# Performance work log

Measured on AMD Instinct MI355X. Metric: run time of the kernel, lower is better.

The kernel has to match this reference:

```python
import jax, jax.numpy as jnp
import numpy as np

B, T, C = 16, 2048, 128
HEAD_SIZE = 128

def setup_inputs() -> dict:
    key = jax.random.key(0)
    k1, k2, k3, k4 = jax.random.split(key, 4)
    x = jax.random.normal(k1, (B, T, C), dtype=jnp.float32)
    # nn.Linear(N_EMBED, head_size, bias=False) weight shape: [head_size, N_EMBED]
    scale = (1.0 / np.sqrt(C)).astype(np.float32)
    Wq = jax.random.normal(k2, (HEAD_SIZE, C), dtype=jnp.float32) * scale
    Wk = jax.random.normal(k3, (HEAD_SIZE, C), dtype=jnp.float32) * scale
    Wv = jax.random.normal(k4, (HEAD_SIZE, C), dtype=jnp.float32) * scale
    return {"x": x, "Wq": Wq, "Wk": Wk, "Wv": Wv}

def reference(x, Wq, Wk, Wv):
    Bd, Td, Cd = x.shape
    q = jnp.einsum('btc,hc->bth', x, Wq)  # [B,T,H]
    k = jnp.einsum('btc,hc->bth', x, Wk)
    v = jnp.einsum('btc,hc->bth', x, Wv)
    # NOTE: original scales by C**-0.5 (embedding dim), not head_size**-0.5
    scores = jnp.einsum('bth,bsh->bts', q, k) * (Cd ** -0.5)  # [B,T,T]
    causal = jnp.tril(jnp.ones((Td, Td), dtype=bool))
    scores = jnp.where(causal, scores, -jnp.inf)
    attn = jax.nn.softmax(scores, axis=-1)
    out = jnp.einsum('bts,bsh->bth', attn, v)  # [B,T,H]
    return out
```

## Files before the change

kernel.cpp:

```cpp
#include <hip/hip_runtime.h>
#include <hip/hip_bf16.h>

#define BB 16
#define TT 2048
#define CC 128
#define HH 128
#define NQT128 16

typedef __bf16 bf16x8 __attribute__((ext_vector_type(8)));
typedef __bf16 bf16x4 __attribute__((ext_vector_type(4)));
typedef float  f32x4  __attribute__((ext_vector_type(4)));
typedef unsigned int u32x2 __attribute__((ext_vector_type(2)));

#define BTH       ((size_t)BB * TT * HH)
#define WBF_OFF   (3 * BTH)

static __device__ __forceinline__ bf16x8 load_cvt8(const float* p) {
    float4 a = *(const float4*)p;
    float4 b = *(const float4*)(p + 4);
    bf16x8 r;
    r[0] = (__bf16)a.x; r[1] = (__bf16)a.y; r[2] = (__bf16)a.z; r[3] = (__bf16)a.w;
    r[4] = (__bf16)b.x; r[5] = (__bf16)b.y; r[6] = (__bf16)b.z; r[7] = (__bf16)b.w;
    return r;
}

static __device__ __forceinline__ void load_lds16(const void* g, void* l) {
    __builtin_amdgcn_global_load_lds(
        (const __attribute__((address_space(1))) unsigned int*)g,
        (__attribute__((address_space(3))) unsigned int*)l, 16, 0, 0);
}

__global__ __launch_bounds__(256) void wcvt_kernel(
    const float* __restrict__ Wq, const float* __restrict__ Wk,
    const float* __restrict__ Wv, __bf16* __restrict__ wbf)
{
    int idx = blockIdx.x * 256 + threadIdx.x;
    int which = idx >> 11;
    int rem = idx & 2047;
    int blk = rem >> 8;
    int r2  = rem & 255;
    int ks   = r2 >> 6;
    int lane = r2 & 63;
    int quad = lane >> 4, l16 = lane & 15;
    const float* src = (which == 0) ? Wq : (which == 1) ? Wk : Wv;
    float sc = (which == 0) ? (0.08838834764831845f * 1.4426950408889634f) : 1.0f;
    const float* p = src + (size_t)(blk * 16 + l16) * CC + ks * 32 + quad * 8;
    bf16x8 v;
    #pragma unroll
    for (int j = 0; j < 8; ++j) v[j] = (__bf16)(p[j] * sc);
    *(bf16x8*)(wbf + (size_t)which * 16384 + (((size_t)(blk * 4 + ks)) << 9) + lane * 8) = v;
}

#define TR_QK 132
#define TR_V  68

__global__ __launch_bounds__(256) void proj_kernel(
    const float* __restrict__ x, __bf16* __restrict__ ws)
{
    __shared__ float  xs[64 * 132];
    __shared__ __bf16 tr[128 * TR_V];

    const int lane = threadIdx.x & 63;
    const int wave = threadIdx.x >> 6;
    const int quad = lane >> 4;
    const int l16  = lane & 15;
    const int tid  = threadIdx.x;
    const int m0 = blockIdx.x * 64;
    const int b  = m0 / TT;
    const int t0 = m0 % TT;

    const __bf16* Wbf = ws + WBF_OFF;
    __bf16* Qs = ws;
    __bf16* Ks = ws + BTH;
    __bf16* Vs = ws + 2 * BTH;

    const float* xg = x + (size_t)m0 * CC;
    #pragma unroll
    for (int t = 0; t < 8; ++t) {
        int f = t * 256 + tid;
        int row = f >> 5, c4 = f & 31;
        float4 v = *(const float4*)(xg + (size_t)f * 4);
        *(float4*)(&xs[row * 132 + c4 * 4]) = v;
    }
    __syncthreads();

    bf16x8 xf[4];
    #pragma unroll
    for (int ks = 0; ks < 4; ++ks)
        xf[ks] = load_cvt8(&xs[(wave * 16 + l16) * 132 + ks * 32 + quad * 8]);

    #pragma unroll
    for (int which = 0; which < 2; ++which) {
        const __bf16* Wb = Wbf + (size_t)which * 16384;
        __bf16* dst = which ? Ks : Qs;
        #pragma unroll
        for (int nt = 0; nt < 8; ++nt) {
            f32x4 acc = {0.f, 0.f, 0.f, 0.f};
            #pragma unroll
            for (int ks = 0; ks < 4; ++ks) {
                bf16x8 wf = *(const bf16x8*)(Wb + (((size_t)(nt * 4 + ks)) << 9) + lane * 8);
                acc = __builtin_amdgcn_mfma_f32_16x16x32_bf16(xf[ks], wf, acc, 0, 0, 0);
            }
            #pragma unroll
            for (int r = 0; r < 4; ++r)
                tr[(wave * 16 + quad * 4 + r) * TR_QK + nt * 16 + l16] = (__bf16)acc[r];
        }
        asm volatile("s_waitcnt lgkmcnt(0)" ::: "memory");
        #pragma unroll
        for (int ks = 0; ks < 4; ++ks) {
            const __bf16* p = &tr[(wave * 16 + l16) * TR_QK + ks * 32 + quad * 8];
            uint2 lo = *(const uint2*)p;
            uint2 hi = *(const uint2*)(p + 4);
            uint4 v; v.x = lo.x; v.y = lo.y; v.z = hi.x; v.w = hi.y;
            __bf16* o = dst + (((size_t)(b * 128 + t0 / 16 + wave) * 4 + ks) << 9) + lane * 8;
            *(uint4*)o = v;
        }
        asm volatile("s_waitcnt lgkmcnt(0)" ::: "memory");
    }

    __syncthreads();
    const __bf16* Wv = Wbf + 2 * 16384;
    #pragma unroll
    for (int msub = 0; msub < 8; ++msub) {
        f32x4 acc = {0.f, 0.f, 0.f, 0.f};
        #pragma unroll
        for (int ks = 0; ks < 4; ++ks) {
            bf16x8 wf = *(const bf16x8*)(Wv + (((size_t)(msub * 4 + ks)) << 9) + lane * 8);
            acc = __builtin_amdgcn_mfma_f32_16x16x32_bf16(wf, xf[ks], acc, 0, 0, 0);
        }
        #pragma unroll
        for (int r = 0; r < 4; ++r)
            tr[(msub * 16 + quad * 4 + r) * TR_V + wave * 16 + l16] = (__bf16)acc[r];
    }
    __syncthreads();
    #pragma unroll
    for (int i = 0; i < 4; ++i) {
        int t32 = i >> 1;
        int h16 = wave * 2 + (i & 1);
        const __bf16* p = &tr[(h16 * 16 + l16) * TR_V + t32 * 32 + quad * 8];
        uint2 lo = *(const uint2*)p;
        uint2 hi = *(const uint2*)(p + 4);
        uint4 v; v.x = lo.x; v.y = lo.y; v.z = hi.x; v.w = hi.y;
        __bf16* o = Vs + (((size_t)(b * 64 + t0 / 32 + t32) * 8 + h16) << 9) + lane * 8;
        *(uint4*)o = v;
    }
}

__global__ __launch_bounds__(256) void attn_kernel(
    const __bf16* __restrict__ ws, float* __restrict__ outp)
{
    __shared__ char ldsBuf[2][24576];

    const int lane = threadIdx.x & 63;
    const int wave = threadIdx.x >> 6;
    const int quad = lane >> 4;
    const int l16  = lane & 15;
    const int lane8 = lane * 8;
    const int lo16 = lane * 16;

    const int lin = blockIdx.x;
    const int b   = (lin & 7) * 2 + ((lin >> 3) & 1);
    const int rest = lin >> 4;
    const int pid  = rest & 7;
    const int hh0  = (rest >> 3) & 1;
    const int mh   = 1 - (rest >> 4);

    const __bf16* Qs = ws;
    const __bf16* Ks = ws + BTH;
    const __bf16* Vs = ws + 2 * BTH;

    const char* kg = (const char*)Ks + (size_t)b * 524288 + wave * 4096 + lo16;
    const char* vg = (const char*)Vs + (size_t)b * 524288 + hh0 * 4096 + wave * 1024 + lo16;

    #define STAGE64(J, BUF)                                                     \
        do {                                                                    \
            char* dK_ = ldsBuf[BUF] + wave * 4096;                              \
            char* dV_ = ldsBuf[BUF] + 16384 + wave * 1024;                      \
            const char* sk_ = kg + (size_t)(J) * 16384;                         \
            _Pragma("unroll")                                                   \
            for (int c_ = 0; c_ < 4; ++c_)                                      \
                load_lds16(sk_ + c_ * 1024, dK_ + c_ * 1024);                   \
            _Pragma("unroll")                                                   \
            for (int h_ = 0; h_ < 2; ++h_)                                      \
                load_lds16(vg + (size_t)(2 * (J) + h_) * 8192, dV_ + h_ * 4096);\
        } while (0)

    #pragma unroll 1
    for (int pass = 0; pass < 2; ++pass) {
        const int qt = pass ? (15 - pid) : pid;
        const int qw = qt * 128 + mh * 64 + wave * 16;
        const int ttw = (qw >> 5) + 1;
        const int nj  = 2 * qt + mh + 1;

        bf16x8 qf[4];
        #pragma unroll
        for (int ks = 0; ks < 4; ++ks)
            qf[ks] = *(const bf16x8*)(Qs + (((size_t)(b * 128 + qt * 8 + mh * 4 + wave) * 4 + ks) << 9) + lane8);

        float l_r = 0.f;
        f32x4 o[4];
        #pragma unroll
        for (int h8 = 0; h8 < 4; ++h8) o[h8] = (f32x4){0.f, 0.f, 0.f, 0.f};

        STAGE64(0, 0);
        asm volatile("s_waitcnt vmcnt(0)" ::: "memory");
        __builtin_amdgcn_s_barrier();

        for (int j = 0; j < nj; ++j) {
            const int cur = j & 1;
            if (j + 1 < nj) STAGE64(j + 1, cur ^ 1);

            #pragma unroll
            for (int half = 0; half < 2; ++half) {
                const int tt = 2 * j + half;
                if (tt >= ttw) continue;
                const char* lk = ldsBuf[cur] + half * 8192;
                const char* lv = ldsBuf[cur] + 16384 + half * 4096;

                f32x4 s2[2];
                #pragma unroll
                for (int nsub = 0; nsub < 2; ++nsub) {
                    bf16x8 kfr[4];
                    #pragma unroll
                    for (int ks = 0; ks < 4; ++ks)
                        kfr[ks] = *(const bf16x8*)(lk + ((nsub * 4 + ks) << 10) + lo16);
                    f32x4 a2 = {0.f, 0.f, 0.f, 0.f};
                    __builtin_amdgcn_s_setprio(1);
                    #pragma unroll
                    for (int ks = 0; ks < 4; ++ks)
                        a2 = __builtin_amdgcn_mfma_f32_16x16x32_bf16(kfr[ks], qf[ks], a2, 0, 0, 0);
                    __builtin_amdgcn_s_setprio(0);
                    s2[nsub] = a2;
                }

                const int k0 = tt * 32;
                unsigned int du[2][2];
                const int qrow = qw + l16;
                if (k0 + 31 > qw) {
                    #pragma unroll
                    for (int nsub = 0; nsub < 2; ++nsub) {
                        const int kb = k0 + nsub * 16 + quad * 4;
                        union { bf16x4 v; unsigned int u[2]; } cv;
                        #pragma unroll
                        for (int r = 0; r < 4; ++r) {
                            float sv = (kb + r > qrow) ? -3e38f : s2[nsub][r];
                            float p = __builtin_amdgcn_exp2f(sv);
                            l_r += p;
                            cv.v[r] = (__bf16)p;
                        }
                        du[nsub][0] = cv.u[0];
                        du[nsub][1] = cv.u[1];
                    }
                } else {
                    #pragma unroll
                    for (int nsub = 0; nsub < 2; ++nsub) {
                        union { bf16x4 v; unsigned int u[2]; } cv;
                        #pragma unroll
                        for (int r = 0; r < 4; ++r) {
                            float p = __builtin_amdgcn_exp2f(s2[nsub][r]);
                            l_r += p;
                            cv.v[r] = (__bf16)p;
                        }
                        du[nsub][0] = cv.u[0];
                        du[nsub][1] = cv.u[1];
                    }
                }

                bf16x8 pf;
                {
                    union { unsigned int u[4]; bf16x8 v; } cc;
                    #pragma unroll
                    for (int h = 0; h < 2; ++h) {
                        u32x2 t1 = __builtin_amdgcn_permlane32_swap(
                            du[0][h], du[1][h], false, false);
                        u32x2 t2 = __builtin_amdgcn_permlane16_swap(
                            t1[0], t1[1], false, false);
                        cc.u[h]     = t2[0];
                        cc.u[2 + h] = t2[1];
                    }
                    pf = cc.v;
                }

                __builtin_amdgcn_s_setprio(1);
                #pragma unroll
                for (int h8 = 0; h8 < 4; ++h8) {
                    bf16x8 v0 = *(const bf16x8*)(lv + (h8 << 10) + lo16);
                    o[h8] = __builtin_amdgcn_mfma_f32_16x16x32_bf16(pf, v0, o[h8], 0, 0, 0);
                }
                __builtin_amdgcn_s_setprio(0);
            }
            asm volatile("s_waitcnt vmcnt(0)" ::: "memory");
            __builtin_amdgcn_s_barrier();
        }

        l_r += __shfl_xor(l_r, 16, 64);
        l_r += __shfl_xor(l_r, 32, 64);
        float inv[4];
        #pragma unroll
        for (int r = 0; r < 4; ++r)
            inv[r] = 1.0f / __shfl(l_r, (lane & 48) | (quad * 4 + r), 64);
        #pragma unroll
        for (int h8 = 0; h8 < 4; ++h8)
            #pragma unroll
            for (int r = 0; r < 4; ++r)
                outp[(size_t)(b * TT + qw + quad * 4 + r) * HH + hh0 * 64 + h8 * 16 + l16] = o[h8][r] * inv[r];
    }
    #undef STAGE64
}

extern "C" void kernel_launch(void* const* d_in, const int* in_sizes, int n_in,
                              void* d_out, int out_size, void* d_ws, size_t ws_size,
                              hipStream_t stream)
{
    const float* x  = (const float*)d_in[0];
    const float* Wq = (const float*)d_in[1];
    const float* Wk = (const float*)d_in[2];
    const float* Wv = (const float*)d_in[3];
    __bf16* ws = (__bf16*)d_ws;
    float* out = (float*)d_out;

    wcvt_kernel<<<24, 256, 0, stream>>>(Wq, Wk, Wv, ws + WBF_OFF);
    proj_kernel<<<512, 256, 0, stream>>>(x, ws);
    attn_kernel<<<512, 256, 0, stream>>>(ws, out);
}
```

Measured before the change: 127.1 us.

## Restructure attention into 2-wave blocks covering one 32-row query tile with full head width

```diff
diff --git a/kernel.cpp b/kernel.cpp
--- a/kernel.cpp
+++ b/kernel.cpp
@@ -146,10 +146,10 @@
     }
 }
 
-__global__ __launch_bounds__(256) void attn_kernel(
+__global__ __launch_bounds__(128) void attn_kernel(
     const __bf16* __restrict__ ws, float* __restrict__ outp)
 {
-    __shared__ char ldsBuf[2][24576];
+    __shared__ char ldsBuf[2][16384];
 
     const int lane = threadIdx.x & 63;
     const int wave = threadIdx.x >> 6;
@@ -160,152 +160,139 @@
 
     const int lin = blockIdx.x;
     const int b   = (lin & 7) * 2 + ((lin >> 3) & 1);
-    const int rest = lin >> 4;
-    const int pid  = rest & 7;
-    const int hh0  = (rest >> 3) & 1;
-    const int mh   = 1 - (rest >> 4);
+    const int kq  = 63 - (lin >> 4);
+    const int qw  = kq * 32 + wave * 16;
+    const int nt  = kq + 1;
 
     const __bf16* Qs = ws;
     const __bf16* Ks = ws + BTH;
     const __bf16* Vs = ws + 2 * BTH;
 
-    const char* kg = (const char*)Ks + (size_t)b * 524288 + wave * 4096 + lo16;
-    const char* vg = (const char*)Vs + (size_t)b * 524288 + hh0 * 4096 + wave * 1024 + lo16;
-
-    #define STAGE64(J, BUF)                                                     \
-        do {                                                                    \
-            char* dK_ = ldsBuf[BUF] + wave * 4096;                              \
-            char* dV_ = ldsBuf[BUF] + 16384 + wave * 1024;                      \
-            const char* sk_ = kg + (size_t)(J) * 16384;                         \
-            _Pragma("unroll")                                                   \
-            for (int c_ = 0; c_ < 4; ++c_)                                      \
-                load_lds16(sk_ + c_ * 1024, dK_ + c_ * 1024);                   \
-            _Pragma("unroll")                                                   \
-            for (int h_ = 0; h_ < 2; ++h_)                                      \
-                load_lds16(vg + (size_t)(2 * (J) + h_) * 8192, dV_ + h_ * 4096);\
+    bf16x8 qf[4];
+    #pragma unroll
+    for (int ks = 0; ks < 4; ++ks)
+        qf[ks] = *(const bf16x8*)(Qs + (((size_t)(b * 128 + 2 * kq + wave) * 4 + ks) << 9) + lane8);
+
+    float l_r = 0.f;
+    f32x4 o[8];
+    #pragma unroll
+    for (int h8 = 0; h8 < 8; ++h8) o[h8] = (f32x4){0.f, 0.f, 0.f, 0.f};
+
+    const char* sbase = (wave ? (const char*)Vs : (const char*)Ks)
+                        + (size_t)b * 524288 + lo16;
+
+    #define STAGE(TTv, BUF)                                        \
+        do {                                                       \
+            const char* s_ = sbase + ((size_t)(TTv) << 13);        \
+            char* d_ = ldsBuf[BUF] + wave * 8192;                  \
+            _Pragma("unroll")                                      \
+            for (int c_ = 0; c_ < 8; ++c_)                         \
+                load_lds16(s_ + c_ * 1024, d_ + c_ * 1024);        \
         } while (0)
 
-    #pragma unroll 1
-    for (int pass = 0; pass < 2; ++pass) {
-        const int qt = pass ? (15 - pid) : pid;
-        const int qw = qt * 128 + mh * 64 + wave * 16;
-        const int ttw = (qw >> 5) + 1;
-        const int nj  = 2 * qt + mh + 1;
-
-        bf16x8 qf[4];
-        #pragma unroll
-        for (int ks = 0; ks < 4; ++ks)
-            qf[ks] = *(const bf16x8*)(Qs + (((size_t)(b * 128 + qt * 8 + mh * 4 + wave) * 4 + ks) << 9) + lane8);
-
-        float l_r = 0.f;
-        f32x4 o[4];
-        #pragma unroll
-        for (int h8 = 0; h8 < 4; ++h8) o[h8] = (f32x4){0.f, 0.f, 0.f, 0.f};
-
-        STAGE64(0, 0);
-        asm volatile("s_waitcnt vmcnt(0)" ::: "memory");
+    STAGE(0, 0);
+
+    for (int tt = 0; tt < nt; ++tt) {
+        const int cur = tt & 1;
+        if (tt + 1 < nt) {
+            STAGE(tt + 1, cur ^ 1);
+            asm volatile("s_waitcnt vmcnt(8)" ::: "memory");
+        } else {
+            asm volatile("s_waitcnt vmcnt(0)" ::: "memory");
+        }
         __builtin_amdgcn_s_barrier();
 
-        for (int j = 0; j < nj; ++j) {
-            const int cur = j & 1;
-            if (j + 1 < nj) STAGE64(j + 1, cur ^ 1);
-
-            #pragma unroll
-            for (int half = 0; half < 2; ++half) {
-                const int tt = 2 * j + half;
-                if (tt >= ttw) continue;
-                const char* lk = ldsBuf[cur] + half * 8192;
-                const char* lv = ldsBuf[cur] + 16384 + half * 4096;
-
-                f32x4 s2[2];
+        const char* lk = ldsBuf[cur];
+        const char* lv = ldsBuf[cur] + 8192;
+
+        f32x4 s2[2];
+        #pragma unroll
+        for (int nsub = 0; nsub < 2; ++nsub) {
+            bf16x8 kfr[4];
+            #pragma unroll
+            for (int ks = 0; ks < 4; ++ks)
+                kfr[ks] = *(const bf16x8*)(lk + ((nsub * 4 + ks) << 10) + lo16);
+            f32x4 a2 = {0.f, 0.f, 0.f, 0.f};
+            __builtin_amdgcn_s_setprio(1);
+            #pragma unroll
+            for (int ks = 0; ks < 4; ++ks)
+                a2 = __builtin_amdgcn_mfma_f32_16x16x32_bf16(kfr[ks], qf[ks], a2, 0, 0, 0);
+            __builtin_amdgcn_s_setprio(0);
+            s2[nsub] = a2;
+        }
+
+        const int k0 = tt * 32;
+        unsigned int du[2][2];
+        if (tt == nt - 1) {
+            const int qrow = qw + l16;
+            #pragma unroll
+            for (int nsub = 0; nsub < 2; ++nsub) {
+                const int kb = k0 + nsub * 16 + quad * 4;
+                union { bf16x4 v; unsigned int u[2]; } cv;
                 #pragma unroll
-                for (int nsub = 0; nsub < 2; ++nsub) {
-                    bf16x8 kfr[4];
-                    #pragma unroll
-                    for (int ks = 0; ks < 4; ++ks)
-                        kfr[ks] = *(const bf16x8*)(lk + ((nsub * 4 + ks) << 10) + lo16);
-                    f32x4 a2 = {0.f, 0.f, 0.f, 0.f};
-                    __builtin_amdgcn_s_setprio(1);
-                    #pragma unroll
-                    for (int ks = 0; ks < 4; ++ks)
-                        a2 = __builtin_amdgcn_mfma_f32_16x16x32_bf16(kfr[ks], qf[ks], a2, 0, 0, 0);
-                    __builtin_amdgcn_s_setprio(0);
-                    s2[nsub] = a2;
+                for (int r = 0; r < 4; ++r) {
+                    float sv = (kb + r > qrow) ? -3e38f : s2[nsub][r];
+                    float p = __builtin_amdgcn_exp2f(sv);
+                    l_r += p;
+                    cv.v[r] = (__bf16)p;
                 }
-
-                const int k0 = tt * 32;
-                unsigned int du[2][2];
-                const int qrow = qw + l16;
-                if (k0 + 31 > qw) {
-                    #pragma unroll
-                    for (int nsub = 0; nsub < 2; ++nsub) {
-                        const int kb = k0 + nsub * 16 + quad * 4;
-                        union { bf16x4 v; unsigned int u[2]; } cv;
-                        #pragma unroll
-                        for (int r = 0; r < 4; ++r) {
-                            float sv = (kb + r > qrow) ? -3e38f : s2[nsub][r];
-                            float p = __builtin_amdgcn_exp2f(sv);
-                            l_r += p;
-                            cv.v[r] = (__bf16)p;
-                        }
-                        du[nsub][0] = cv.u[0];
-                        du[nsub][1] = cv.u[1];
-                    }
-                } else {
-                    #pragma unroll
-                    for (int nsub = 0; nsub < 2; ++nsub) {
-                        union { bf16x4 v; unsigned int u[2]; } cv;
-                        #pragma unroll
-                        for (int r = 0; r < 4; ++r) {
-                            float p = __builtin_amdgcn_exp2f(s2[nsub][r]);
-                            l_r += p;
-                            cv.v[r] = (__bf16)p;
-                        }
-                        du[nsub][0] = cv.u[0];
-                        du[nsub][1] = cv.u[1];
-                    }
+                du[nsub][0] = cv.u[0];
+                du[nsub][1] = cv.u[1];
+            }
+        } else {
+            #pragma unroll
+            for (int nsub = 0; nsub < 2; ++nsub) {
+                union { bf16x4 v; unsigned int u[2]; } cv;
+                #pragma unroll
+                for (int r = 0; r < 4; ++r) {
+                    float p = __builtin_amdgcn_exp2f(s2[nsub][r]);
+                    l_r += p;
+                    cv.v[r] = (__bf16)p;
                 }
-
-                bf16x8 pf;
-                {
-                    union { unsigned int u[4]; bf16x8 v; } cc;
-                    #pragma unroll
-                    for (int h = 0; h < 2; ++h) {
-                        u32x2 t1 = __builtin_amdgcn_permlane32_swap(
-                            du[0][h], du[1][h], false, false);
-                        u32x2 t2 = __builtin_amdgcn_permlane16_swap(
-                            t1[0], t1[1], false, false);
-                        cc.u[h]     = t2[0];
-                        cc.u[2 + h] = t2[1];
-                    }
-                    pf = cc.v;
-                }
-
-                __builtin_amdgcn_s_setprio(1);
-                #pragma unroll
-                for (int h8 = 0; h8 < 4; ++h8) {
-                    bf16x8 v0 = *(const bf16x8*)(lv + (h8 << 10) + lo16);
-                    o[h8] = __builtin_amdgcn_mfma_f32_16x16x32_bf16(pf, v0, o[h8], 0, 0, 0);
-                }
-                __builtin_amdgcn_s_setprio(0);
+                du[nsub][0] = cv.u[0];
+                du[nsub][1] = cv.u[1];
             }
-            asm volatile("s_waitcnt vmcnt(0)" ::: "memory");
-            __builtin_amdgcn_s_barrier();
-        }
-
-        l_r += __shfl_xor(l_r, 16, 64);
-        l_r += __shfl_xor(l_r, 32, 64);
-        float inv[4];
+        }
+
+        bf16x8 pf;
+        {
+            union { unsigned int u[4]; bf16x8 v; } cc;
+            #pragma unroll
+            for (int h = 0; h < 2; ++h) {
+                u32x2 t1 = __builtin_amdgcn_permlane32_swap(
+                    du[0][h], du[1][h], false, false);
+                u32x2 t2 = __builtin_amdgcn_permlane16_swap(
+                    t1[0], t1[1], false, false);
+                cc.u[h]     = t2[0];
+                cc.u[2 + h] = t2[1];
+            }
+            pf = cc.v;
+        }
+
+        __builtin_amdgcn_s_setprio(1);
+        #pragma unroll
+        for (int h8 = 0; h8 < 8; ++h8) {
+            bf16x8 v0 = *(const bf16x8*)(lv + (h8 << 10) + lo16);
+            o[h8] = __builtin_amdgcn_mfma_f32_16x16x32_bf16(pf, v0, o[h8], 0, 0, 0);
+        }
+        __builtin_amdgcn_s_setprio(0);
+
+        asm volatile("s_waitcnt lgkmcnt(0)" ::: "memory");
+        __builtin_amdgcn_s_barrier();
+    }
+    #undef STAGE
+
+    l_r += __shfl_xor(l_r, 16, 64);
+    l_r += __shfl_xor(l_r, 32, 64);
+    float inv[4];
+    #pragma unroll
+    for (int r = 0; r < 4; ++r)
+        inv[r] = 1.0f / __shfl(l_r, (lane & 48) | (quad * 4 + r), 64);
+    #pragma unroll
+    for (int h8 = 0; h8 < 8; ++h8)
         #pragma unroll
         for (int r = 0; r < 4; ++r)
-            inv[r] = 1.0f / __shfl(l_r, (lane & 48) | (quad * 4 + r), 64);
-        #pragma unroll
-        for (int h8 = 0; h8 < 4; ++h8)
-            #pragma unroll
-            for (int r = 0; r < 4; ++r)
-                outp[(size_t)(b * TT + qw + quad * 4 + r) * HH + hh0 * 64 + h8 * 16 + l16] = o[h8][r] * inv[r];
-    }
-    #undef STAGE64
+            outp[(size_t)(b * TT + qw + quad * 4 + r) * HH + h8 * 16 + l16] = o[h8][r] * inv[r];
 }
 
 extern "C" void kernel_launch(void* const* d_in, const int* in_sizes, int n_in,
@@ -321,5 +308,5 @@
 
     wcvt_kernel<<<24, 256, 0, stream>>>(Wq, Wk, Wv, ws + WBF_OFF);
     proj_kernel<<<512, 256, 0, stream>>>(x, ws);
-    attn_kernel<<<512, 256, 0, stream>>>(ws, out);
-}
+    attn_kernel<<<1024, 128, 0, stream>>>(ws, out);
+}
```

Measured after the change: 123.7 us. 1.03x faster.
